# Optimization experiments

Measured on AMD Instinct MI355X. Metric: run time of the kernel, lower is better.

The kernel has to match this reference:

```python
import jax, jax.numpy as jnp
import numpy as np

N_LEVELS = 16
F_PER = 2
LOG2_T = 19
T = 1 << LOG2_T            # 524288 hash table entries per level
BASE = 32
SCALE = 1.3819
RES = 512
CLAMP = 25.133             # sine pre-activation clamp (8*pi)
N = 1 << 19                # number of query points
RESOLUTIONS = np.floor(BASE * SCALE ** np.arange(N_LEVELS)).astype(np.int32)
PRIME = np.uint32(2654435761)


def _hash2d(ix, iy):
    # instant-NGP style spatial hash for 2D integer coords -> [0, T)
    return ((ix.astype(jnp.uint32) ^ (iy.astype(jnp.uint32) * PRIME)) & jnp.uint32(T - 1)).astype(jnp.int32)


def hashgrid_lookup(uv, table):
    # uv: [N,2] in [0,1]; table: [L, T, F]. Returns [N, L*F].
    feats = []
    for l in range(N_LEVELS):
        res = int(RESOLUTIONS[l])
        pos = uv * (res - 1)                         # [N,2]
        p0 = jnp.floor(pos)
        f = pos - p0                                 # fractional part [N,2]
        x0 = p0[:, 0].astype(jnp.int32)
        y0 = p0[:, 1].astype(jnp.int32)
        x1 = jnp.minimum(x0 + 1, res - 1)
        y1 = jnp.minimum(y0 + 1, res - 1)
        tab = table[l]                               # [T, F]
        c00 = tab[_hash2d(x0, y0)]
        c10 = tab[_hash2d(x1, y0)]
        c01 = tab[_hash2d(x0, y1)]
        c11 = tab[_hash2d(x1, y1)]
        fx = f[:, 0:1]
        fy = f[:, 1:2]
        feats.append(c00 * (1 - fx) * (1 - fy) + c10 * fx * (1 - fy)
                     + c01 * (1 - fx) * fy + c11 * fx * fy)
    return jnp.concatenate(feats, axis=-1)           # [N, 32]


def siren(h, w, b):
    return jnp.sin(jnp.clip(h @ w.T + b, -CLAMP, CLAMP))


def setup_inputs() -> dict:
    key = jax.random.key(0)
    ks = jax.random.split(key, 8)
    y = jax.random.uniform(ks[0], (N,), jnp.float32, 0.0, RES - 1)
    x = jax.random.uniform(ks[1], (N,), jnp.float32, 0.0, RES - 1)
    cam_feat = jax.random.normal(ks[2], (N, 32), jnp.float32)
    table = jax.random.uniform(ks[3], (N_LEVELS, T, F_PER), jnp.float32, -1e-4, 1e-4)
    d_in = 64
    w1 = jax.random.uniform(ks[4], (512, d_in), jnp.float32, -1.0 / d_in, 1.0 / d_in)
    b1 = jnp.zeros((512,), jnp.float32)
    w2 = jax.random.uniform(ks[5], (512, 512), jnp.float32, -1.0 / 512, 1.0 / 512)
    b2 = jnp.zeros((512,), jnp.float32)
    w3 = jax.random.uniform(ks[6], (384, 512), jnp.float32, -1.0 / 512, 1.0 / 512)
    b3 = jnp.zeros((384,), jnp.float32)
    return {"y": y, "x": x, "cam_feat": cam_feat, "table": table,
            "w1": w1, "b1": b1, "w2": w2, "b2": b2, "w3": w3, "b3": b3}


def reference(y, x, cam_feat, table, w1, b1, w2, b2, w3, b3):
    # uv = [x,y] clamped to [0, RES-1] then normalized to [0,1]
    uv = jnp.stack([jnp.clip(x, 0.0, RES - 1) / (RES - 1),
                    jnp.clip(y, 0.0, RES - 1) / (RES - 1)], axis=-1)  # [N,2]
    codes = hashgrid_lookup(uv, table)                # [N,32]
    h = jnp.concatenate([codes, cam_feat], axis=-1)   # [N,64]
    h = siren(h, w1, b1)
    h = siren(h, w2, b2)
    return siren(h, w3, b3)                           # [N,384]
```

## Files before the change

### kernel.cpp

```cpp
#include <hip/hip_runtime.h>
#include <math.h>

#define NLEV 16
#define TSIZE (1u << 19)
#define PRIME 2654435761u
#define CLAMP_V 25.133f
#define MT 64
#define SH_STRIDE 72
#define SA_STRIDE 520

typedef _Float16 half8_t __attribute__((ext_vector_type(8)));
typedef float f32x4 __attribute__((ext_vector_type(4)));

#define W1_ENT 0
#define W2_ENT 4096
#define W3_ENT (4096 + 32768)
#define N_ENT (4096 + 32768 + 24576)

struct ResTab { int r[NLEV]; };

__device__ __forceinline__ float fast_sin(float v) {
    float n = rintf(v * 0.31830988618367f);
    float r = fmaf(n, -3.14159274101257f, v);
    r = fmaf(n, 8.742278012618954e-8f, r);
    float r2 = r * r;
    float p = fmaf(r2, -2.5050760253e-8f, 2.7557313707e-6f);
    p = fmaf(r2, p, -1.9841269830e-4f);
    p = fmaf(r2, p, 8.3333333333e-3f);
    p = fmaf(r2, p, -1.6666666667e-1f);
    float s = fmaf(r * r2, p, r);
    int ni = (int)n;
    return (ni & 1) ? -s : s;
}

__device__ __forceinline__ float act(float v, float bias) {
    v += bias;
    v = fminf(fmaxf(v, -CLAMP_V), CLAMP_V);
    return fast_sin(v);
}

__global__ void prep_weights(const float* __restrict__ w1, const float* __restrict__ w2,
                             const float* __restrict__ w3, _Float16* __restrict__ pack) {
    int tid = blockIdx.x * 256 + threadIdx.x;
    if (tid >= N_ENT) return;
    const float* src;
    int K, NT, e;
    if (tid < W2_ENT)      { src = w1; K = 64;  NT = 32; e = tid; }
    else if (tid < W3_ENT) { src = w2; K = 512; NT = 32; e = tid - W2_ENT; }
    else                   { src = w3; K = 512; NT = 24; e = tid - W3_ENT; }
    int lane = e & 63;
    int rest = e >> 6;
    int t = rest % NT, kk = rest / NT;
    int nn = t * 16 + (lane & 15);
    int k0 = kk * 32 + (lane >> 4) * 8;
    const float* s = src + (size_t)nn * K + k0;
    _Float16* d = pack + (size_t)tid * 8;
#pragma unroll
    for (int j = 0; j < 8; j++) d[j] = (_Float16)s[j];
}

__launch_bounds__(256, 2)
__global__ void fused_mlp(const float* __restrict__ gy, const float* __restrict__ gx,
                          const float* __restrict__ cam, const float* __restrict__ table,
                          const float* __restrict__ b1, const float* __restrict__ b2,
                          const float* __restrict__ b3, const _Float16* __restrict__ pack,
                          float* __restrict__ out, ResTab rt) {
    __shared__ _Float16 sH[MT * SH_STRIDE];
    __shared__ _Float16 sA[MT * SA_STRIDE];
    const int tid = threadIdx.x;
    const int r0 = blockIdx.x * MT;

    {
        const int lev = tid & 15;
        const int rbase = tid >> 4;
        const int res = rt.r[lev];
        const float fres = (float)(res - 1);
        const int rmax = res - 1;
        const float2* tab = ((const float2*)table) + (size_t)lev * TSIZE;
#pragma unroll
        for (int i = 0; i < 4; i++) {
            const int row = rbase + i * 16;
            const int rr = r0 + row;
            float xx = fminf(fmaxf(gx[rr], 0.0f), 511.0f) / 511.0f;
            float yy = fminf(fmaxf(gy[rr], 0.0f), 511.0f) / 511.0f;
            float px = xx * fres, py = yy * fres;
            float p0x = floorf(px), p0y = floorf(py);
            float fx = px - p0x, fy = py - p0y;
            int x0 = (int)p0x, y0 = (int)p0y;
            int x1 = min(x0 + 1, rmax), y1 = min(y0 + 1, rmax);
            unsigned hy0 = (unsigned)y0 * PRIME, hy1 = (unsigned)y1 * PRIME;
            unsigned ux0 = (unsigned)x0, ux1 = (unsigned)x1;
            float2 c00 = tab[(ux0 ^ hy0) & (TSIZE - 1)];
            float2 c10 = tab[(ux1 ^ hy0) & (TSIZE - 1)];
            float2 c01 = tab[(ux0 ^ hy1) & (TSIZE - 1)];
            float2 c11 = tab[(ux1 ^ hy1) & (TSIZE - 1)];
            float w00 = (1.0f - fx) * (1.0f - fy), w10 = fx * (1.0f - fy);
            float w01 = (1.0f - fx) * fy, w11 = fx * fy;
            float f0 = c00.x * w00 + c10.x * w10 + c01.x * w01 + c11.x * w11;
            float f1 = c00.y * w00 + c10.y * w10 + c01.y * w01 + c11.y * w11;
            union { _Float16 h[2]; unsigned u; } pk;
            pk.h[0] = (_Float16)f0; pk.h[1] = (_Float16)f1;
            *(unsigned*)&sH[row * SH_STRIDE + 2 * lev] = pk.u;
        }
        const float4* cf = (const float4*)cam;
#pragma unroll
        for (int i = 0; i < 2; i++) {
            int e = tid + i * 256;
            float4 v = cf[(size_t)r0 * 8 + e];
            int row = e >> 3, c4 = (e & 7) * 4;
            _Float16* d = &sH[row * SH_STRIDE + 32 + c4];
            d[0] = (_Float16)v.x; d[1] = (_Float16)v.y;
            d[2] = (_Float16)v.z; d[3] = (_Float16)v.w;
        }
    }
    __syncthreads();

    const int wv = tid >> 6, lane = tid & 63, ln = lane & 15, q = lane >> 4;
    const half8_t* packv = (const half8_t*)pack;
    const f32x4 vzero = {0.0f, 0.0f, 0.0f, 0.0f};

    {
        f32x4 acc[4][8];
#pragma unroll
        for (int mb = 0; mb < 4; mb++)
#pragma unroll
            for (int nt = 0; nt < 8; nt++) acc[mb][nt] = vzero;
#pragma unroll
        for (int kk = 0; kk < 2; kk++) {
            half8_t a[4];
#pragma unroll
            for (int mb = 0; mb < 4; mb++)
                a[mb] = *(const half8_t*)&sH[(mb * 16 + ln) * SH_STRIDE + kk * 32 + q * 8];
#pragma unroll
            for (int nt = 0; nt < 8; nt++) {
                half8_t b = packv[W1_ENT + (kk * 32 + wv * 8 + nt) * 64 + lane];
#pragma unroll
                for (int mb = 0; mb < 4; mb++)
                    acc[mb][nt] = __builtin_amdgcn_mfma_f32_16x16x32_f16(a[mb], b, acc[mb][nt], 0, 0, 0);
            }
        }
#pragma unroll
        for (int nt = 0; nt < 8; nt++) {
            int n = wv * 128 + nt * 16 + ln;
            float bias = b1[n];
#pragma unroll
            for (int mb = 0; mb < 4; mb++)
#pragma unroll
                for (int r = 0; r < 4; r++) {
                    int m = mb * 16 + q * 4 + r;
                    sA[m * SA_STRIDE + n] = (_Float16)act(acc[mb][nt][r], bias);
                }
        }
    }
    __syncthreads();

    {
        f32x4 acc[4][8];
#pragma unroll
        for (int mb = 0; mb < 4; mb++)
#pragma unroll
            for (int nt = 0; nt < 8; nt++) acc[mb][nt] = vzero;
        for (int kk = 0; kk < 16; kk++) {
            half8_t a[4];
#pragma unroll
            for (int mb = 0; mb < 4; mb++)
                a[mb] = *(const half8_t*)&sA[(mb * 16 + ln) * SA_STRIDE + kk * 32 + q * 8];
#pragma unroll
            for (int nt = 0; nt < 8; nt++) {
                half8_t b = packv[W2_ENT + (kk * 32 + wv * 8 + nt) * 64 + lane];
#pragma unroll
                for (int mb = 0; mb < 4; mb++)
                    acc[mb][nt] = __builtin_amdgcn_mfma_f32_16x16x32_f16(a[mb], b, acc[mb][nt], 0, 0, 0);
            }
        }
        __syncthreads();
#pragma unroll
        for (int nt = 0; nt < 8; nt++) {
            int n = wv * 128 + nt * 16 + ln;
            float bias = b2[n];
#pragma unroll
            for (int mb = 0; mb < 4; mb++)
#pragma unroll
                for (int r = 0; r < 4; r++) {
                    int m = mb * 16 + q * 4 + r;
                    sA[m * SA_STRIDE + n] = (_Float16)act(acc[mb][nt][r], bias);
                }
        }
    }
    __syncthreads();

    {
        f32x4 acc[4][6];
#pragma unroll
        for (int mb = 0; mb < 4; mb++)
#pragma unroll
            for (int nt = 0; nt < 6; nt++) acc[mb][nt] = vzero;
        for (int kk = 0; kk < 16; kk++) {
            half8_t a[4];
#pragma unroll
            for (int mb = 0; mb < 4; mb++)
                a[mb] = *(const half8_t*)&sA[(mb * 16 + ln) * SA_STRIDE + kk * 32 + q * 8];
#pragma unroll
            for (int nt = 0; nt < 6; nt++) {
                half8_t b = packv[W3_ENT + (kk * 24 + wv * 6 + nt) * 64 + lane];
#pragma unroll
                for (int mb = 0; mb < 4; mb++)
                    acc[mb][nt] = __builtin_amdgcn_mfma_f32_16x16x32_f16(a[mb], b, acc[mb][nt], 0, 0, 0);
            }
        }
#pragma unroll
        for (int nt = 0; nt < 6; nt++) {
            int n = wv * 96 + nt * 16 + ln;
            float bias = b3[n];
#pragma unroll
            for (int mb = 0; mb < 4; mb++)
#pragma unroll
                for (int r = 0; r < 4; r++) {
                    int m = mb * 16 + q * 4 + r;
                    out[(size_t)(r0 + m) * 384 + n] = act(acc[mb][nt][r], bias);
                }
        }
    }
}

extern "C" void kernel_launch(void* const* d_in, const int* in_sizes, int n_in,
                              void* d_out, int out_size, void* d_ws, size_t ws_size,
                              hipStream_t stream) {
    const float* y   = (const float*)d_in[0];
    const float* x   = (const float*)d_in[1];
    const float* cam = (const float*)d_in[2];
    const float* tab = (const float*)d_in[3];
    const float* w1  = (const float*)d_in[4];
    const float* b1  = (const float*)d_in[5];
    const float* w2  = (const float*)d_in[6];
    const float* b2  = (const float*)d_in[7];
    const float* w3  = (const float*)d_in[8];
    const float* b3  = (const float*)d_in[9];
    float* out = (float*)d_out;
    _Float16* pack = (_Float16*)d_ws;

    ResTab rt;
    for (int l = 0; l < NLEV; l++)
        rt.r[l] = (int)floor(32.0 * pow(1.3819, (double)l));

    prep_weights<<<dim3((N_ENT + 255) / 256), dim3(256), 0, stream>>>(w1, w2, w3, pack);

    int nblocks = in_sizes[0] / MT;
    fused_mlp<<<dim3(nblocks), dim3(256), 0, stream>>>(y, x, cam, tab, b1, b2, b3,
                                                       (const _Float16*)pack, out, rt);
}
```

Measured before the change: 1.769 ms.

## Use 512-thread blocks, transposed MFMA outputs, hardware sin with pre-scaled weights

Doubles the block to 512 threads (8 waves), so each wave owns half as many output columns and the per-wave accumulator footprint shrinks, which should raise occupancy. It swaps the MFMA operand order so every lane holds four consecutive output columns, allowing packed 8-byte stores to LDS and float4 stores to global memory. It folds 1/(2π) into W1, W2 and their biases and uses the hardware sin instruction on range-reduced revolutions for the hidden layers. Biases now initialise the accumulators instead of being added afterwards. The hardware sin and the fp16 weight scaling may reduce accuracy slightly.

Measured after the change: 1.504 ms. -15.0%, faster.

```diff
diff --git a/kernel.cpp b/kernel.cpp
--- a/kernel.cpp
+++ b/kernel.cpp
@@ -5,6 +5,8 @@
 #define TSIZE (1u << 19)
 #define PRIME 2654435761u
 #define CLAMP_V 25.133f
+#define INV_2PI 0.15915494309189535f
+#define CLAMP_REV 4.0000420f
 #define MT 64
 #define SH_STRIDE 72
 #define SA_STRIDE 520
@@ -33,10 +35,10 @@
     return (ni & 1) ? -s : s;
 }
 
-__device__ __forceinline__ float act(float v, float bias) {
-    v += bias;
-    v = fminf(fmaxf(v, -CLAMP_V), CLAMP_V);
-    return fast_sin(v);
+__device__ __forceinline__ _Float16 hsin(float m) {
+    m = fminf(fmaxf(m, -CLAMP_REV), CLAMP_REV);
+    float t = m - rintf(m);
+    return (_Float16)__builtin_amdgcn_sinf(t);
 }
 
 __global__ void prep_weights(const float* __restrict__ w1, const float* __restrict__ w2,
@@ -45,9 +47,10 @@
     if (tid >= N_ENT) return;
     const float* src;
     int K, NT, e;
-    if (tid < W2_ENT)      { src = w1; K = 64;  NT = 32; e = tid; }
-    else if (tid < W3_ENT) { src = w2; K = 512; NT = 32; e = tid - W2_ENT; }
-    else                   { src = w3; K = 512; NT = 24; e = tid - W3_ENT; }
+    float scl;
+    if (tid < W2_ENT)      { src = w1; K = 64;  NT = 32; e = tid;          scl = INV_2PI; }
+    else if (tid < W3_ENT) { src = w2; K = 512; NT = 32; e = tid - W2_ENT; scl = INV_2PI; }
+    else                   { src = w3; K = 512; NT = 24; e = tid - W3_ENT; scl = 1.0f;   }
     int lane = e & 63;
     int rest = e >> 6;
     int t = rest % NT, kk = rest / NT;
@@ -56,10 +59,10 @@
     const float* s = src + (size_t)nn * K + k0;
     _Float16* d = pack + (size_t)tid * 8;
 #pragma unroll
-    for (int j = 0; j < 8; j++) d[j] = (_Float16)s[j];
-}
-
-__launch_bounds__(256, 2)
+    for (int j = 0; j < 8; j++) d[j] = (_Float16)(s[j] * scl);
+}
+
+__launch_bounds__(512, 4)
 __global__ void fused_mlp(const float* __restrict__ gy, const float* __restrict__ gx,
                           const float* __restrict__ cam, const float* __restrict__ table,
                           const float* __restrict__ b1, const float* __restrict__ b2,
@@ -78,8 +81,8 @@
         const int rmax = res - 1;
         const float2* tab = ((const float2*)table) + (size_t)lev * TSIZE;
 #pragma unroll
-        for (int i = 0; i < 4; i++) {
-            const int row = rbase + i * 16;
+        for (int i = 0; i < 2; i++) {
+            const int row = rbase + i * 32;
             const int rr = r0 + row;
             float xx = fminf(fmaxf(gx[rr], 0.0f), 511.0f) / 511.0f;
             float yy = fminf(fmaxf(gy[rr], 0.0f), 511.0f) / 511.0f;
@@ -103,28 +106,27 @@
             *(unsigned*)&sH[row * SH_STRIDE + 2 * lev] = pk.u;
         }
         const float4* cf = (const float4*)cam;
-#pragma unroll
-        for (int i = 0; i < 2; i++) {
-            int e = tid + i * 256;
-            float4 v = cf[(size_t)r0 * 8 + e];
-            int row = e >> 3, c4 = (e & 7) * 4;
-            _Float16* d = &sH[row * SH_STRIDE + 32 + c4];
-            d[0] = (_Float16)v.x; d[1] = (_Float16)v.y;
-            d[2] = (_Float16)v.z; d[3] = (_Float16)v.w;
-        }
+        float4 v = cf[(size_t)r0 * 8 + tid];
+        int row = tid >> 3, c4 = (tid & 7) * 4;
+        _Float16* d = &sH[row * SH_STRIDE + 32 + c4];
+        d[0] = (_Float16)v.x; d[1] = (_Float16)v.y;
+        d[2] = (_Float16)v.z; d[3] = (_Float16)v.w;
     }
     __syncthreads();
 
     const int wv = tid >> 6, lane = tid & 63, ln = lane & 15, q = lane >> 4;
     const half8_t* packv = (const half8_t*)pack;
-    const f32x4 vzero = {0.0f, 0.0f, 0.0f, 0.0f};
-
-    {
-        f32x4 acc[4][8];
-#pragma unroll
-        for (int mb = 0; mb < 4; mb++)
-#pragma unroll
-            for (int nt = 0; nt < 8; nt++) acc[mb][nt] = vzero;
+
+
+    {
+        f32x4 acc[4][4];
+#pragma unroll
+        for (int nt = 0; nt < 4; nt++) {
+            const float4 bb = *(const float4*)(b1 + (wv * 64 + nt * 16 + q * 4));
+            f32x4 bi = {bb.x * INV_2PI, bb.y * INV_2PI, bb.z * INV_2PI, bb.w * INV_2PI};
+#pragma unroll
+            for (int mb = 0; mb < 4; mb++) acc[mb][nt] = bi;
+        }
 #pragma unroll
         for (int kk = 0; kk < 2; kk++) {
             half8_t a[4];
@@ -132,93 +134,105 @@
             for (int mb = 0; mb < 4; mb++)
                 a[mb] = *(const half8_t*)&sH[(mb * 16 + ln) * SH_STRIDE + kk * 32 + q * 8];
 #pragma unroll
-            for (int nt = 0; nt < 8; nt++) {
-                half8_t b = packv[W1_ENT + (kk * 32 + wv * 8 + nt) * 64 + lane];
+            for (int nt = 0; nt < 4; nt++) {
+                half8_t b = packv[W1_ENT + (kk * 32 + wv * 4 + nt) * 64 + lane];
 #pragma unroll
                 for (int mb = 0; mb < 4; mb++)
-                    acc[mb][nt] = __builtin_amdgcn_mfma_f32_16x16x32_f16(a[mb], b, acc[mb][nt], 0, 0, 0);
-            }
-        }
-#pragma unroll
-        for (int nt = 0; nt < 8; nt++) {
-            int n = wv * 128 + nt * 16 + ln;
-            float bias = b1[n];
-#pragma unroll
-            for (int mb = 0; mb < 4; mb++)
-#pragma unroll
-                for (int r = 0; r < 4; r++) {
-                    int m = mb * 16 + q * 4 + r;
-                    sA[m * SA_STRIDE + n] = (_Float16)act(acc[mb][nt][r], bias);
-                }
+                    acc[mb][nt] = __builtin_amdgcn_mfma_f32_16x16x32_f16(b, a[mb], acc[mb][nt], 0, 0, 0);
+            }
+        }
+#pragma unroll
+        for (int nt = 0; nt < 4; nt++) {
+            const int n0 = wv * 64 + nt * 16 + q * 4;
+#pragma unroll
+            for (int mb = 0; mb < 4; mb++) {
+                union { _Float16 h[4]; uint2 u; } pk;
+#pragma unroll
+                for (int r = 0; r < 4; r++) pk.h[r] = hsin(acc[mb][nt][r]);
+                *(uint2*)&sA[(mb * 16 + ln) * SA_STRIDE + n0] = pk.u;
+            }
         }
     }
     __syncthreads();
 
     {
-        f32x4 acc[4][8];
-#pragma unroll
-        for (int mb = 0; mb < 4; mb++)
-#pragma unroll
-            for (int nt = 0; nt < 8; nt++) acc[mb][nt] = vzero;
+        f32x4 acc[4][4];
+#pragma unroll
+        for (int nt = 0; nt < 4; nt++) {
+            const float4 bb = *(const float4*)(b2 + (wv * 64 + nt * 16 + q * 4));
+            f32x4 bi = {bb.x * INV_2PI, bb.y * INV_2PI, bb.z * INV_2PI, bb.w * INV_2PI};
+#pragma unroll
+            for (int mb = 0; mb < 4; mb++) acc[mb][nt] = bi;
+        }
         for (int kk = 0; kk < 16; kk++) {
             half8_t a[4];
 #pragma unroll
             for (int mb = 0; mb < 4; mb++)
                 a[mb] = *(const half8_t*)&sA[(mb * 16 + ln) * SA_STRIDE + kk * 32 + q * 8];
 #pragma unroll
-            for (int nt = 0; nt < 8; nt++) {
-                half8_t b = packv[W2_ENT + (kk * 32 + wv * 8 + nt) * 64 + lane];
+            for (int nt = 0; nt < 4; nt++) {
+                half8_t b = packv[W2_ENT + (kk * 32 + wv * 4 + nt) * 64 + lane];
 #pragma unroll
                 for (int mb = 0; mb < 4; mb++)
-                    acc[mb][nt] = __builtin_amdgcn_mfma_f32_16x16x32_f16(a[mb], b, acc[mb][nt], 0, 0, 0);
-            }
-        }
+                    acc[mb][nt] = __builtin_amdgcn_mfma_f32_16x16x32_f16(b, a[mb], acc[mb][nt], 0, 0, 0);
+            }
+        }
+        uint2 pk[4][4];
+#pragma unroll
+        for (int nt = 0; nt < 4; nt++)
+#pragma unroll
+            for (int mb = 0; mb < 4; mb++) {
+                union { _Float16 h[4]; uint2 u; } t;
+#pragma unroll
+                for (int r = 0; r < 4; r++) t.h[r] = hsin(acc[mb][nt][r]);
+                pk[nt][mb] = t.u;
+            }
         __syncthreads();
 #pragma unroll
-        for (int nt = 0; nt < 8; nt++) {
-            int n = wv * 128 + nt * 16 + ln;
-            float bias = b2[n];
-#pragma unroll
-            for (int mb = 0; mb < 4; mb++)
-#pragma unroll
-                for (int r = 0; r < 4; r++) {
-                    int m = mb * 16 + q * 4 + r;
-                    sA[m * SA_STRIDE + n] = (_Float16)act(acc[mb][nt][r], bias);
-                }
+        for (int nt = 0; nt < 4; nt++) {
+            const int n0 = wv * 64 + nt * 16 + q * 4;
+#pragma unroll
+            for (int mb = 0; mb < 4; mb++)
+                *(uint2*)&sA[(mb * 16 + ln) * SA_STRIDE + n0] = pk[nt][mb];
         }
     }
     __syncthreads();
 
     {
-        f32x4 acc[4][6];
-#pragma unroll
-        for (int mb = 0; mb < 4; mb++)
-#pragma unroll
-            for (int nt = 0; nt < 6; nt++) acc[mb][nt] = vzero;
+        f32x4 acc[4][3];
+#pragma unroll
+        for (int nt = 0; nt < 3; nt++) {
+            const float4 bb = *(const float4*)(b3 + (wv * 48 + nt * 16 + q * 4));
+            f32x4 bi = {bb.x, bb.y, bb.z, bb.w};
+#pragma unroll
+            for (int mb = 0; mb < 4; mb++) acc[mb][nt] = bi;
+        }
         for (int kk = 0; kk < 16; kk++) {
             half8_t a[4];
 #pragma unroll
             for (int mb = 0; mb < 4; mb++)
                 a[mb] = *(const half8_t*)&sA[(mb * 16 + ln) * SA_STRIDE + kk * 32 + q * 8];
 #pragma unroll
-            for (int nt = 0; nt < 6; nt++) {
-                half8_t b = packv[W3_ENT + (kk * 24 + wv * 6 + nt) * 64 + lane];
+            for (int nt = 0; nt < 3; nt++) {
+                half8_t b = packv[W3_ENT + (kk * 24 + wv * 3 + nt) * 64 + lane];
 #pragma unroll
                 for (int mb = 0; mb < 4; mb++)
-                    acc[mb][nt] = __builtin_amdgcn_mfma_f32_16x16x32_f16(a[mb], b, acc[mb][nt], 0, 0, 0);
-            }
-        }
-#pragma unroll
-        for (int nt = 0; nt < 6; nt++) {
-            int n = wv * 96 + nt * 16 + ln;
-            float bias = b3[n];
-#pragma unroll
-            for (int mb = 0; mb < 4; mb++)
-#pragma unroll
-                for (int r = 0; r < 4; r++) {
-                    int m = mb * 16 + q * 4 + r;
-                    out[(size_t)(r0 + m) * 384 + n] = act(acc[mb][nt][r], bias);
-                }
+                    acc[mb][nt] = __builtin_amdgcn_mfma_f32_16x16x32_f16(b, a[mb], acc[mb][nt], 0, 0, 0);
+            }
+        }
+#pragma unroll
+        for (int nt = 0; nt < 3; nt++) {
+            const int n0 = wv * 48 + nt * 16 + q * 4;
+#pragma unroll
+            for (int mb = 0; mb < 4; mb++) {
+                float4 o;
+                float vv;
+                vv = fminf(fmaxf(acc[mb][nt][0], -CLAMP_V), CLAMP_V); o.x = fast_sin(vv);
+                vv = fminf(fmaxf(acc[mb][nt][1], -CLAMP_V), CLAMP_V); o.y = fast_sin(vv);
+                vv = fminf(fmaxf(acc[mb][nt][2], -CLAMP_V), CLAMP_V); o.z = fast_sin(vv);
+                vv = fminf(fmaxf(acc[mb][nt][3], -CLAMP_V), CLAMP_V); o.w = fast_sin(vv);
+                *(float4*)&out[(size_t)(r0 + mb * 16 + ln) * 384 + n0] = o;
+            }
         }
     }
 }
@@ -246,6 +260,6 @@
     prep_weights<<<dim3((N_ENT + 255) / 256), dim3(256), 0, stream>>>(w1, w2, w3, pack);
 
     int nblocks = in_sizes[0] / MT;
-    fused_mlp<<<dim3(nblocks), dim3(256), 0, stream>>>(y, x, cam, tab, b1, b2, b3,
+    fused_mlp<<<dim3(nblocks), dim3(512), 0, stream>>>(y, x, cam, tab, b1, b2, b3,
                                                        (const _Float16*)pack, out, rt);
 }
```
